# Kernel tuning notes

Hardware: AMD Instinct MI355X
Metric: run time of the kernel (lower is better)

The kernel has to match this reference:

```python
import jax, jax.numpy as jnp
import numpy as np

N = 100_000   # nodes
E = 1_600_000 # edges
D = 128       # feat_dim
H = 128       # hidden dim (both layers)
L = 64        # latent dim
BN_EPS = 1e-5


def setup_inputs() -> dict:
    key = jax.random.key(0)
    ks = jax.random.split(key, 16)
    x = jax.random.normal(ks[0], (N, D), dtype=jnp.float32)
    edge_index = jax.random.randint(ks[1], (2, E), 0, N, dtype=jnp.int64)
    s = 0.05
    return {
        "x": x,
        "edge_index": edge_index,
        # GCN layer 1
        "W1": jax.random.normal(ks[2], (D, H), dtype=jnp.float32) * s,
        "b1": jnp.zeros((H,), dtype=jnp.float32),
        "g1": jnp.ones((H,), dtype=jnp.float32),
        "be1": jnp.zeros((H,), dtype=jnp.float32),
        # GCN layer 2
        "W2": jax.random.normal(ks[3], (H, H), dtype=jnp.float32) * s,
        "b2": jnp.zeros((H,), dtype=jnp.float32),
        "g2": jnp.ones((H,), dtype=jnp.float32),
        "be2": jnp.zeros((H,), dtype=jnp.float32),
        # heads
        "Wmu": jax.random.normal(ks[4], (H, L), dtype=jnp.float32) * s,
        "bmu": jnp.zeros((L,), dtype=jnp.float32),
        "Wlv": jax.random.normal(ks[5], (H, L), dtype=jnp.float32) * s,
        "blv": jnp.zeros((L,), dtype=jnp.float32),
    }


def _gcn_conv(h, src, dst, deg_isqrt, W, b):
    # PyG GCNConv: linear first, then D^{-1/2}(A+I)D^{-1/2} aggregation, then bias.
    hW = h @ W                                   # [N, H]
    norm = deg_isqrt[src] * deg_isqrt[dst]       # [E]
    msg = hW[src] * norm[:, None]                # gather + scale, [E, H]
    agg = jax.ops.segment_sum(msg, dst, num_segments=N)
    # self-loop contribution (norm = deg_isqrt[i]^2)
    agg = agg + hW * (deg_isqrt * deg_isqrt)[:, None]
    return agg + b


def _bn_relu(h, g, be):
    # training-mode BatchNorm1d over the node dim (biased variance), then ReLU
    mean = jnp.mean(h, axis=0)
    var = jnp.mean(jnp.square(h - mean), axis=0)
    hn = (h - mean) * jax.lax.rsqrt(var + BN_EPS) * g + be
    return jax.nn.relu(hn)


def reference(x, edge_index, W1, b1, g1, be1, W2, b2, g2, be2, Wmu, bmu, Wlv, blv):
    src, dst = edge_index[0], edge_index[1]
    # degree with self loops (computed on destination nodes)
    deg = jax.ops.segment_sum(jnp.ones((E,), dtype=x.dtype), dst, num_segments=N) + 1.0
    deg_isqrt = jax.lax.rsqrt(deg)

    h = _bn_relu(_gcn_conv(x, src, dst, deg_isqrt, W1, b1), g1, be1)
    h = _bn_relu(_gcn_conv(h, src, dst, deg_isqrt, W2, b2), g2, be2)
    # dropout is identity in eval mode
    mu = h @ Wmu + bmu
    logvar = h @ Wlv + blv
    return mu, logvar
```

## Files before the change

### kernel.cpp

```cpp
#include <hip/hip_runtime.h>


typedef __attribute__((ext_vector_type(8))) short bf16x8;
typedef __attribute__((ext_vector_type(4))) float f32x4;

#define NB   256
#define PSZ  256
#define PMAX 512

__device__ inline unsigned short f2bf(float f) {
    unsigned u = __float_as_uint(f);
    unsigned r = u + 0x7FFFu + ((u >> 16) & 1u);
    return (unsigned short)(r >> 16);
}
__device__ inline float bf2f(unsigned u16) {
    return __uint_as_float(u16 << 16);
}

__global__ void k_edetect(const int* __restrict__ ei, int n, int* __restrict__ flag) {
    if (threadIdx.x == 0 && blockIdx.x == 0) {
        int is64 = 1;
        for (int i = 0; i < 64; ++i) {
            if (ei[2 * i + 1] != 0 || (unsigned)ei[2 * i] >= (unsigned)n) { is64 = 0; break; }
        }
        *flag = is64;
    }
}

__device__ inline void load_edge(const int* __restrict__ ei, int eflag, size_t i, size_t e,
                                 int& s, int& d) {
    if (eflag) {
        s = ei[2 * i];
        d = ei[2 * e + 2 * i];
    } else {
        s = ei[i];
        d = ei[e + i];
    }
}


__global__ __launch_bounds__(256) void k_hist(const int* __restrict__ ei,
                                              const int* __restrict__ eflag,
                                              unsigned* __restrict__ gh,
                                              int e, int n, int P, int epb) {
    __shared__ unsigned hist[PMAX];
    int t = threadIdx.x, b = blockIdx.x;
    for (int p = t; p < P; p += 256) hist[p] = 0u;
    __syncthreads();
    int f = *eflag;
    int end = min(e, (b + 1) * epb);
    for (int i = b * epb + t; i < end; i += 256) {
        int s, d;
        load_edge(ei, f, (size_t)i, (size_t)e, s, d);
        if ((unsigned)d < (unsigned)n) atomicAdd(&hist[d >> 8], 1u);
    }
    __syncthreads();
    for (int p = t; p < P; p += 256) gh[(size_t)p * NB + b] = hist[p];
}


__global__ __launch_bounds__(256) void k_scanp(const unsigned* __restrict__ gh,
                                               unsigned* __restrict__ boffs,
                                               unsigned* __restrict__ tot, int P) {
    __shared__ unsigned tmp[256];
    int p = blockIdx.x, t = threadIdx.x;
    unsigned v = gh[(size_t)p * NB + t];
    tmp[t] = v;
    __syncthreads();
    for (int o = 1; o < 256; o <<= 1) {
        unsigned u = (t >= o) ? tmp[t - o] : 0u;
        __syncthreads();
        tmp[t] += u;
        __syncthreads();
    }
    boffs[(size_t)p * NB + t] = tmp[t] - v;
    if (t == 255) tot[p] = tmp[255];
}


__global__ void k_scant(const unsigned* __restrict__ tot,
                        unsigned* __restrict__ gofs, int P) {
    __shared__ unsigned tmp[512];
    int t = threadIdx.x;
    unsigned v = (t < P) ? tot[t] : 0u;
    tmp[t] = v;
    __syncthreads();
    for (int o = 1; o < 512; o <<= 1) {
        unsigned u = (t >= o) ? tmp[t - o] : 0u;
        __syncthreads();
        tmp[t] += u;
        __syncthreads();
    }
    if (t < P) gofs[t] = tmp[t] - v;
}


__global__ __launch_bounds__(256) void k_stage(const int* __restrict__ ei,
                                               const int* __restrict__ eflag,
                                               const unsigned* __restrict__ boffs,
                                               const unsigned* __restrict__ gofs,
                                               uint2* __restrict__ staged,
                                               int e, int n, int P, int epb) {
    __shared__ unsigned cur[PMAX];
    int t = threadIdx.x, b = blockIdx.x;
    for (int p = t; p < P; p += 256) cur[p] = gofs[p] + boffs[(size_t)p * NB + b];
    __syncthreads();
    int f = *eflag;
    int end = min(e, (b + 1) * epb);
    for (int i = b * epb + t; i < end; i += 256) {
        int s, d;
        load_edge(ei, f, (size_t)i, (size_t)e, s, d);
        if ((unsigned)d >= (unsigned)n) continue;
        unsigned pos = atomicAdd(&cur[d >> 8], 1u);
        if (pos < (unsigned)e) staged[pos] = make_uint2((unsigned)s, (unsigned)d);
    }
}


__global__ __launch_bounds__(256) void k_fill(const uint2* __restrict__ staged,
                                              const unsigned* __restrict__ gofs,
                                              const unsigned* __restrict__ tot,
                                              int* __restrict__ csr_src,
                                              unsigned* __restrict__ deg,
                                              float* __restrict__ dis,
                                              unsigned* __restrict__ starts,
                                              int n, int P) {
    __shared__ unsigned h2[256], tmp[256], cur2[256];
    int p = blockIdx.x, t = threadIdx.x;
    unsigned base = gofs[p], cnt = tot[p];
    h2[t] = 0u;
    __syncthreads();
    for (unsigned i = t; i < cnt; i += 256) {
        unsigned dl = staged[base + i].y & 255u;
        atomicAdd(&h2[dl], 1u);
    }
    __syncthreads();
    unsigned cv = h2[t];
    tmp[t] = cv;
    __syncthreads();
    for (int o = 1; o < 256; o <<= 1) {
        unsigned u = (t >= o) ? tmp[t - o] : 0u;
        __syncthreads();
        tmp[t] += u;
        __syncthreads();
    }
    unsigned excl = tmp[t] - cv;
    int node = p * PSZ + t;
    if (node < n) {
        deg[node]    = cv;
        dis[node]    = rsqrtf((float)cv + 1.0f);
        starts[node] = base + excl;
    }
    cur2[t] = base + excl;
    __syncthreads();
    for (unsigned i = t; i < cnt; i += 256) {
        uint2 ed = staged[base + i];
        unsigned slot = atomicAdd(&cur2[ed.y & 255u], 1u);
        csr_src[slot] = (ed.x < (unsigned)n) ? (int)ed.x : 0;
    }
}


__global__ __launch_bounds__(256) void prep_weights(const float* __restrict__ W1,
                                                    const float* __restrict__ W2,
                                                    const float* __restrict__ Wmu,
                                                    const float* __restrict__ Wlv,
                                                    const float* __restrict__ bmu,
                                                    const float* __restrict__ blv,
                                                    unsigned short* __restrict__ Wt1,
                                                    unsigned short* __restrict__ Wt2,
                                                    unsigned short* __restrict__ Wtc,
                                                    float* __restrict__ bcat) {
    int idx = blockIdx.x * 256 + threadIdx.x;
    if (idx < 16384) {
        int c = idx >> 7, k = idx & 127;
        Wt1[idx] = f2bf(W1[(size_t)k * 128 + c]);
    } else if (idx < 32768) {
        int t = idx - 16384, c = t >> 7, k = t & 127;
        Wt2[t] = f2bf(W2[(size_t)k * 128 + c]);
    } else if (idx < 49152) {
        int t = idx - 32768, c = t >> 7, k = t & 127;
        float v = (c < 64) ? Wmu[(size_t)k * 64 + c] : Wlv[(size_t)k * 64 + (c - 64)];
        Wtc[t] = f2bf(v);
    }
    if (idx < 128) bcat[idx] = (idx < 64) ? bmu[idx] : blv[idx - 64];
}


__global__ __launch_bounds__(256) void aggregate(const unsigned* __restrict__ hWb,
                                                 const int* __restrict__ csr_src,
                                                 const unsigned* __restrict__ starts,
                                                 const unsigned* __restrict__ deg,
                                                 const float* __restrict__ dis,
                                                 const float* __restrict__ bias,
                                                 float* __restrict__ outh, int n) {
    int node = blockIdx.x * 4 + (threadIdx.x >> 6);
    int lane = threadIdx.x & 63;
    if (node >= n) return;
    unsigned s0 = starts[node], dn = deg[node];
    float ax = 0.f, ay = 0.f;
    unsigned j = 0;
    for (; j + 16 <= dn; j += 16) {
        int si[16]; unsigned vv[16]; float ww[16];
#pragma unroll
        for (int q = 0; q < 16; ++q) si[q] = csr_src[s0 + j + q];
#pragma unroll
        for (int q = 0; q < 16; ++q) vv[q] = hWb[(size_t)si[q] * 64 + lane];
#pragma unroll
        for (int q = 0; q < 16; ++q) ww[q] = dis[si[q]];
#pragma unroll
        for (int q = 0; q < 16; ++q) {
            ax = fmaf(bf2f(vv[q] & 0xFFFFu), ww[q], ax);
            ay = fmaf(bf2f(vv[q] >> 16), ww[q], ay);
        }
    }
    for (; j + 8 <= dn; j += 8) {
        int si[8]; unsigned vv[8]; float ww[8];
#pragma unroll
        for (int q = 0; q < 8; ++q) si[q] = csr_src[s0 + j + q];
#pragma unroll
        for (int q = 0; q < 8; ++q) vv[q] = hWb[(size_t)si[q] * 64 + lane];
#pragma unroll
        for (int q = 0; q < 8; ++q) ww[q] = dis[si[q]];
#pragma unroll
        for (int q = 0; q < 8; ++q) {
            ax = fmaf(bf2f(vv[q] & 0xFFFFu), ww[q], ax);
            ay = fmaf(bf2f(vv[q] >> 16), ww[q], ay);
        }
    }
    for (; j + 4 <= dn; j += 4) {
        int si[4]; unsigned vv[4]; float ww[4];
#pragma unroll
        for (int q = 0; q < 4; ++q) si[q] = csr_src[s0 + j + q];
#pragma unroll
        for (int q = 0; q < 4; ++q) vv[q] = hWb[(size_t)si[q] * 64 + lane];
#pragma unroll
        for (int q = 0; q < 4; ++q) ww[q] = dis[si[q]];
#pragma unroll
        for (int q = 0; q < 4; ++q) {
            ax = fmaf(bf2f(vv[q] & 0xFFFFu), ww[q], ax);
            ay = fmaf(bf2f(vv[q] >> 16), ww[q], ay);
        }
    }
    for (; j < dn; ++j) {
        int      s = csr_src[s0 + j];
        float    w = dis[s];
        unsigned v = hWb[(size_t)s * 64 + lane];
        ax = fmaf(bf2f(v & 0xFFFFu), w, ax);
        ay = fmaf(bf2f(v >> 16), w, ay);
    }
    float dii = dis[node];
    unsigned vs = hWb[(size_t)node * 64 + lane];
    float rx = fmaf(dii, ax, dii * dii * bf2f(vs & 0xFFFFu)) + bias[lane * 2];
    float ry = fmaf(dii, ay, dii * dii * bf2f(vs >> 16)) + bias[lane * 2 + 1];
    *(float2*)(outh + (size_t)node * 128 + lane * 2) = make_float2(rx, ry);
}


__global__ __launch_bounds__(256) void bn_stats(const float* __restrict__ h,
                                                float* __restrict__ sums, int n) {
    int tid = threadIdx.x;
    int c = tid & 127, half = tid >> 7;
    float s = 0.f, s2 = 0.f;
    for (int r = blockIdx.x * 2 + half; r < n; r += gridDim.x * 2) {
        float v = h[(size_t)r * 128 + c];
        s += v;
        s2 = fmaf(v, v, s2);
    }
    __shared__ float sh[256];
    sh[tid] = s;
    __syncthreads();
    if (tid < 128) atomicAdd(&sums[tid], sh[tid] + sh[tid + 128]);
    __syncthreads();
    sh[tid] = s2;
    __syncthreads();
    if (tid < 128) atomicAdd(&sums[128 + tid], sh[tid] + sh[tid + 128]);
}

__global__ void bn_final(const float* __restrict__ sums, const float* __restrict__ g,
                         const float* __restrict__ be, float* __restrict__ bnp, int n) {
    int c = threadIdx.x;
    float inv_n = 1.0f / (float)n;
    float mean = sums[c] * inv_n;
    float var  = sums[128 + c] * inv_n - mean * mean;
    float sc   = g[c] * rsqrtf(var + 1e-5f);
    bnp[c]       = sc;
    bnp[128 + c] = be[c] - mean * sc;
}


template <bool HEAD>
__global__ __launch_bounds__(256, 4) void gemm_mfma(const float* __restrict__ A,
                                                    const unsigned short* __restrict__ Wt,
                                                    const float* __restrict__ bnp,
                                                    const float* __restrict__ bias,
                                                    void* __restrict__ Cv, int nrows) {
    __shared__ float Cl[64][130];
    __shared__ float bnsc[128], bnsh[128];

    const int tid  = threadIdx.x;
    const int lane = tid & 63;
    const int wv   = tid >> 6;
    const int rowbase = blockIdx.x * 64;
    const bool has_bn = (bnp != nullptr);
    if (has_bn && tid < 128) {
        bnsc[tid] = bnp[tid];
        bnsh[tid] = bnp[128 + tid];
    }
    __syncthreads();

    const int ar = rowbase + wv * 16 + (lane & 15);
    const int kg = (lane >> 4) * 8;
    const int bc = lane & 15;

    f32x4 acc[8];
#pragma unroll
    for (int t = 0; t < 8; ++t) acc[t] = {0.f, 0.f, 0.f, 0.f};

#pragma unroll
    for (int k0 = 0; k0 < 128; k0 += 32) {
        float va[8];
        if (ar < nrows) {
            float4 a0 = *(const float4*)(A + (size_t)ar * 128 + k0 + kg);
            float4 a1 = *(const float4*)(A + (size_t)ar * 128 + k0 + kg + 4);
            va[0] = a0.x; va[1] = a0.y; va[2] = a0.z; va[3] = a0.w;
            va[4] = a1.x; va[5] = a1.y; va[6] = a1.z; va[7] = a1.w;
        } else {
#pragma unroll
            for (int i = 0; i < 8; ++i) va[i] = 0.f;
        }
        if (has_bn) {
#pragma unroll
            for (int i = 0; i < 8; ++i) {
                int k = k0 + kg + i;
                va[i] = fmaxf(0.f, fmaf(va[i], bnsc[k], bnsh[k]));
            }
        }
        bf16x8 af;
#pragma unroll
        for (int i = 0; i < 8; ++i) af[i] = (short)f2bf(va[i]);

#pragma unroll
        for (int ct = 0; ct < 8; ++ct) {
            bf16x8 bf = *(const bf16x8*)(Wt + (size_t)(ct * 16 + bc) * 128 + k0 + kg);
            acc[ct] = __builtin_amdgcn_mfma_f32_16x16x32_bf16(af, bf, acc[ct], 0, 0, 0);
        }
    }

    const int lr = wv * 16 + ((lane >> 4) << 2);
#pragma unroll
    for (int ct = 0; ct < 8; ++ct)
#pragma unroll
        for (int r = 0; r < 4; ++r)
            Cl[lr + r][ct * 16 + bc] = acc[ct][r];
    __syncthreads();

    const int row = tid >> 2;
    const int c0  = (tid & 3) * 32;
    const int gr  = rowbase + row;
    if (gr < nrows) {
        if (!HEAD) {
            unsigned* C = (unsigned*)Cv;
#pragma unroll
            for (int u = 0; u < 4; ++u) {
                int cb = c0 + u * 8;
                unsigned o0 = (unsigned)f2bf(Cl[row][cb + 0]) | ((unsigned)f2bf(Cl[row][cb + 1]) << 16);
                unsigned o1 = (unsigned)f2bf(Cl[row][cb + 2]) | ((unsigned)f2bf(Cl[row][cb + 3]) << 16);
                unsigned o2 = (unsigned)f2bf(Cl[row][cb + 4]) | ((unsigned)f2bf(Cl[row][cb + 5]) << 16);
                unsigned o3 = (unsigned)f2bf(Cl[row][cb + 6]) | ((unsigned)f2bf(Cl[row][cb + 7]) << 16);
                uint4 o4 = {o0, o1, o2, o3};
                *(uint4*)(C + (size_t)gr * 64 + cb / 2) = o4;
            }
        } else {
            float* mu = (float*)Cv;
            float* lv = mu + (size_t)nrows * 64;
            float* dst = (c0 < 64) ? (mu + (size_t)gr * 64 + c0) : (lv + (size_t)gr * 64 + (c0 - 64));
#pragma unroll
            for (int u = 0; u < 8; ++u) {
                int cb = c0 + u * 4;
                float4 o = make_float4(Cl[row][cb + 0] + bias[cb + 0],
                                       Cl[row][cb + 1] + bias[cb + 1],
                                       Cl[row][cb + 2] + bias[cb + 2],
                                       Cl[row][cb + 3] + bias[cb + 3]);
                *(float4*)(dst + u * 4) = o;
            }
        }
    }
}


extern "C" void kernel_launch(void* const* d_in, const int* in_sizes, int n_in,
                              void* d_out, int out_size, void* d_ws, size_t ws_size,
                              hipStream_t stream) {
    const float* x   = (const float*)d_in[0];
    const int*   ei  = (const int*)d_in[1];
    const float* W1  = (const float*)d_in[2];
    const float* b1  = (const float*)d_in[3];
    const float* g1  = (const float*)d_in[4];
    const float* be1 = (const float*)d_in[5];
    const float* W2  = (const float*)d_in[6];
    const float* b2  = (const float*)d_in[7];
    const float* g2  = (const float*)d_in[8];
    const float* be2 = (const float*)d_in[9];
    const float* Wmu = (const float*)d_in[10];
    const float* bmu = (const float*)d_in[11];
    const float* Wlv = (const float*)d_in[12];
    const float* blv = (const float*)d_in[13];

    const int n = in_sizes[0] / 128;
    const int e = in_sizes[1] / 2;

    const int P   = (n + PSZ - 1) / PSZ;
    const int epb = (e + NB - 1) / NB;

    char* ws = (char*)d_ws;
    size_t off = 0;
    auto alloc = [&](size_t bytes) {
        void* p = ws + off;
        off = (off + bytes + 255) & ~(size_t)255;
        return p;
    };
    float*          bufH    = (float*)alloc((size_t)n * 128 * 4);
    unsigned*       hWb     = (unsigned*)alloc((size_t)n * 64 * 4);
    uint2*          staged  = (uint2*)alloc((size_t)e * 8);
    int*            csr_src = (int*)alloc((size_t)e * 4);
    unsigned*       gh      = (unsigned*)alloc((size_t)P * NB * 4);
    unsigned*       boffs   = (unsigned*)alloc((size_t)P * NB * 4);
    unsigned*       tot     = (unsigned*)alloc((size_t)P * 4);
    unsigned*       gofs    = (unsigned*)alloc((size_t)P * 4);
    unsigned*       deg     = (unsigned*)alloc((size_t)n * 4);
    float*          dis     = (float*)alloc((size_t)n * 4);
    unsigned*       starts  = (unsigned*)alloc((size_t)n * 4);
    int*            eflag   = (int*)alloc(256);
    float*          sums    = (float*)alloc(256 * 4);
    float*          bnp     = (float*)alloc(256 * 4);
    unsigned short* Wt1     = (unsigned short*)alloc(16384 * 2);
    unsigned short* Wt2     = (unsigned short*)alloc(16384 * 2);
    unsigned short* Wtc     = (unsigned short*)alloc(16384 * 2);
    float*          bcat    = (float*)alloc(128 * 4);

    const int ab = (n + 3) / 4;
    const int gg = (n + 63) / 64;

    prep_weights<<<192, 256, 0, stream>>>(W1, W2, Wmu, Wlv, bmu, blv, Wt1, Wt2, Wtc, bcat);
    k_edetect<<<1, 64, 0, stream>>>(ei, n, eflag);
    k_hist <<<NB, 256, 0, stream>>>(ei, eflag, gh, e, n, P, epb);
    k_scanp<<<P, 256, 0, stream>>>(gh, boffs, tot, P);
    k_scant<<<1, 512, 0, stream>>>(tot, gofs, P);
    k_stage<<<NB, 256, 0, stream>>>(ei, eflag, boffs, gofs, staged, e, n, P, epb);
    k_fill <<<P, 256, 0, stream>>>(staged, gofs, tot, csr_src, deg, dis, starts, n, P);

    gemm_mfma<false><<<gg, 256, 0, stream>>>(x, Wt1, nullptr, nullptr, hWb, n);
    aggregate<<<ab, 256, 0, stream>>>(hWb, csr_src, starts, deg, dis, b1, bufH, n);
    hipMemsetAsync(sums, 0, 1024, stream);
    bn_stats<<<512, 256, 0, stream>>>(bufH, sums, n);
    bn_final<<<1, 128, 0, stream>>>(sums, g1, be1, bnp, n);

    gemm_mfma<false><<<gg, 256, 0, stream>>>(bufH, Wt2, bnp, nullptr, hWb, n);
    aggregate<<<ab, 256, 0, stream>>>(hWb, csr_src, starts, deg, dis, b2, bufH, n);
    hipMemsetAsync(sums, 0, 1024, stream);
    bn_stats<<<512, 256, 0, stream>>>(bufH, sums, n);
    bn_final<<<1, 128, 0, stream>>>(sums, g2, be2, bnp, n);

    gemm_mfma<true><<<gg, 256, 0, stream>>>(bufH, Wtc, bnp, bcat, d_out, n);
}
```

Baseline: 447.5 us.

## Pre-scale GEMM output by source deg^-1/2 and vectorize BN stats

The per-node deg^-1/2 factor is folded into the bf16 output of the feature GEMM, so aggregation becomes a plain sum of gathered rows, with the self term added and a single multiply by the destination factor at the end. This removes the per-edge random gather of dis[src] and the per-edge multiply. Separately, the BatchNorm statistics kernel now reads float4 per thread across 8 row slices and reduces through shared memory. Rounding changes slightly because the scale is applied before bf16 conversion.

```diff
diff --git a/kernel.cpp b/kernel.cpp
--- a/kernel.cpp
+++ b/kernel.cpp
@@ -201,80 +201,85 @@
     float ax = 0.f, ay = 0.f;
     unsigned j = 0;
     for (; j + 16 <= dn; j += 16) {
-        int si[16]; unsigned vv[16]; float ww[16];
+        int si[16]; unsigned vv[16];
 #pragma unroll
         for (int q = 0; q < 16; ++q) si[q] = csr_src[s0 + j + q];
 #pragma unroll
         for (int q = 0; q < 16; ++q) vv[q] = hWb[(size_t)si[q] * 64 + lane];
 #pragma unroll
-        for (int q = 0; q < 16; ++q) ww[q] = dis[si[q]];
-#pragma unroll
         for (int q = 0; q < 16; ++q) {
-            ax = fmaf(bf2f(vv[q] & 0xFFFFu), ww[q], ax);
-            ay = fmaf(bf2f(vv[q] >> 16), ww[q], ay);
+            ax += bf2f(vv[q] & 0xFFFFu);
+            ay += bf2f(vv[q] >> 16);
         }
     }
     for (; j + 8 <= dn; j += 8) {
-        int si[8]; unsigned vv[8]; float ww[8];
+        int si[8]; unsigned vv[8];
 #pragma unroll
         for (int q = 0; q < 8; ++q) si[q] = csr_src[s0 + j + q];
 #pragma unroll
         for (int q = 0; q < 8; ++q) vv[q] = hWb[(size_t)si[q] * 64 + lane];
 #pragma unroll
-        for (int q = 0; q < 8; ++q) ww[q] = dis[si[q]];
-#pragma unroll
         for (int q = 0; q < 8; ++q) {
-            ax = fmaf(bf2f(vv[q] & 0xFFFFu), ww[q], ax);
-            ay = fmaf(bf2f(vv[q] >> 16), ww[q], ay);
+            ax += bf2f(vv[q] & 0xFFFFu);
+            ay += bf2f(vv[q] >> 16);
         }
     }
     for (; j + 4 <= dn; j += 4) {
-        int si[4]; unsigned vv[4]; float ww[4];
+        int si[4]; unsigned vv[4];
 #pragma unroll
         for (int q = 0; q < 4; ++q) si[q] = csr_src[s0 + j + q];
 #pragma unroll
         for (int q = 0; q < 4; ++q) vv[q] = hWb[(size_t)si[q] * 64 + lane];
 #pragma unroll
-        for (int q = 0; q < 4; ++q) ww[q] = dis[si[q]];
-#pragma unroll
         for (int q = 0; q < 4; ++q) {
-            ax = fmaf(bf2f(vv[q] & 0xFFFFu), ww[q], ax);
-            ay = fmaf(bf2f(vv[q] >> 16), ww[q], ay);
+            ax += bf2f(vv[q] & 0xFFFFu);
+            ay += bf2f(vv[q] >> 16);
         }
     }
     for (; j < dn; ++j) {
-        int      s = csr_src[s0 + j];
-        float    w = dis[s];
-        unsigned v = hWb[(size_t)s * 64 + lane];
-        ax = fmaf(bf2f(v & 0xFFFFu), w, ax);
-        ay = fmaf(bf2f(v >> 16), w, ay);
-    }
+        unsigned v = hWb[(size_t)csr_src[s0 + j] * 64 + lane];
+        ax += bf2f(v & 0xFFFFu);
+        ay += bf2f(v >> 16);
+    }
+    unsigned vs = hWb[(size_t)node * 64 + lane];
+    ax += bf2f(vs & 0xFFFFu);
+    ay += bf2f(vs >> 16);
     float dii = dis[node];
-    unsigned vs = hWb[(size_t)node * 64 + lane];
-    float rx = fmaf(dii, ax, dii * dii * bf2f(vs & 0xFFFFu)) + bias[lane * 2];
-    float ry = fmaf(dii, ay, dii * dii * bf2f(vs >> 16)) + bias[lane * 2 + 1];
+    float rx = fmaf(dii, ax, bias[lane * 2]);
+    float ry = fmaf(dii, ay, bias[lane * 2 + 1]);
     *(float2*)(outh + (size_t)node * 128 + lane * 2) = make_float2(rx, ry);
 }
 
 
 __global__ __launch_bounds__(256) void bn_stats(const float* __restrict__ h,
                                                 float* __restrict__ sums, int n) {
-    int tid = threadIdx.x;
-    int c = tid & 127, half = tid >> 7;
-    float s = 0.f, s2 = 0.f;
-    for (int r = blockIdx.x * 2 + half; r < n; r += gridDim.x * 2) {
-        float v = h[(size_t)r * 128 + c];
-        s += v;
-        s2 = fmaf(v, v, s2);
-    }
-    __shared__ float sh[256];
-    sh[tid] = s;
-    __syncthreads();
-    if (tid < 128) atomicAdd(&sums[tid], sh[tid] + sh[tid + 128]);
-    __syncthreads();
-    sh[tid] = s2;
-    __syncthreads();
-    if (tid < 128) atomicAdd(&sums[128 + tid], sh[tid] + sh[tid + 128]);
+    int t  = threadIdx.x;
+    int q  = t & 31;
+    int sl = t >> 5;
+    float s0 = 0.f, s1 = 0.f, s2 = 0.f, s3 = 0.f;
+    float q0 = 0.f, q1 = 0.f, q2 = 0.f, q3 = 0.f;
+    for (int r = blockIdx.x * 8 + sl; r < n; r += gridDim.x * 8) {
+        float4 v = *(const float4*)(h + (size_t)r * 128 + q * 4);
+        s0 += v.x; q0 = fmaf(v.x, v.x, q0);
+        s1 += v.y; q1 = fmaf(v.y, v.y, q1);
+        s2 += v.z; q2 = fmaf(v.z, v.z, q2);
+        s3 += v.w; q3 = fmaf(v.w, v.w, q3);
+    }
+    __shared__ float sh[256][8];
+    sh[t][0] = s0; sh[t][1] = s1; sh[t][2] = s2; sh[t][3] = s3;
+    sh[t][4] = q0; sh[t][5] = q1; sh[t][6] = q2; sh[t][7] = q3;
+    __syncthreads();
+    if (t < 128) {
+        int cq = t >> 2, ce = t & 3;
+        float a = 0.f, b = 0.f;
+#pragma unroll
+        for (int s8 = 0; s8 < 8; ++s8) {
+            a += sh[s8 * 32 + cq][ce];
+            b += sh[s8 * 32 + cq][4 + ce];
+        }
+        atomicAdd(&sums[t], a);
+        atomicAdd(&sums[128 + t], b);
+    }
 }
 
 __global__ void bn_final(const float* __restrict__ sums, const float* __restrict__ g,
@@ -294,6 +299,7 @@
                                                     const unsigned short* __restrict__ Wt,
                                                     const float* __restrict__ bnp,
                                                     const float* __restrict__ bias,
+                                                    const float* __restrict__ disv,
                                                     void* __restrict__ Cv, int nrows) {
     __shared__ float Cl[64][130];
     __shared__ float bnsc[128], bnsh[128];
@@ -360,14 +366,15 @@
     const int gr  = rowbase + row;
     if (gr < nrows) {
         if (!HEAD) {
+            float dsc = disv[gr];
             unsigned* C = (unsigned*)Cv;
 #pragma unroll
             for (int u = 0; u < 4; ++u) {
                 int cb = c0 + u * 8;
-                unsigned o0 = (unsigned)f2bf(Cl[row][cb + 0]) | ((unsigned)f2bf(Cl[row][cb + 1]) << 16);
-                unsigned o1 = (unsigned)f2bf(Cl[row][cb + 2]) | ((unsigned)f2bf(Cl[row][cb + 3]) << 16);
-                unsigned o2 = (unsigned)f2bf(Cl[row][cb + 4]) | ((unsigned)f2bf(Cl[row][cb + 5]) << 16);
-                unsigned o3 = (unsigned)f2bf(Cl[row][cb + 6]) | ((unsigned)f2bf(Cl[row][cb + 7]) << 16);
+                unsigned o0 = (unsigned)f2bf(Cl[row][cb + 0] * dsc) | ((unsigned)f2bf(Cl[row][cb + 1] * dsc) << 16);
+                unsigned o1 = (unsigned)f2bf(Cl[row][cb + 2] * dsc) | ((unsigned)f2bf(Cl[row][cb + 3] * dsc) << 16);
+                unsigned o2 = (unsigned)f2bf(Cl[row][cb + 4] * dsc) | ((unsigned)f2bf(Cl[row][cb + 5] * dsc) << 16);
+                unsigned o3 = (unsigned)f2bf(Cl[row][cb + 6] * dsc) | ((unsigned)f2bf(Cl[row][cb + 7] * dsc) << 16);
                 uint4 o4 = {o0, o1, o2, o3};
                 *(uint4*)(C + (size_t)gr * 64 + cb / 2) = o4;
             }
@@ -450,17 +457,17 @@
     k_stage<<<NB, 256, 0, stream>>>(ei, eflag, boffs, gofs, staged, e, n, P, epb);
     k_fill <<<P, 256, 0, stream>>>(staged, gofs, tot, csr_src, deg, dis, starts, n, P);
 
-    gemm_mfma<false><<<gg, 256, 0, stream>>>(x, Wt1, nullptr, nullptr, hWb, n);
+    gemm_mfma<false><<<gg, 256, 0, stream>>>(x, Wt1, nullptr, nullptr, dis, hWb, n);
     aggregate<<<ab, 256, 0, stream>>>(hWb, csr_src, starts, deg, dis, b1, bufH, n);
     hipMemsetAsync(sums, 0, 1024, stream);
     bn_stats<<<512, 256, 0, stream>>>(bufH, sums, n);
     bn_final<<<1, 128, 0, stream>>>(sums, g1, be1, bnp, n);
 
-    gemm_mfma<false><<<gg, 256, 0, stream>>>(bufH, Wt2, bnp, nullptr, hWb, n);
+    gemm_mfma<false><<<gg, 256, 0, stream>>>(bufH, Wt2, bnp, nullptr, dis, hWb, n);
     aggregate<<<ab, 256, 0, stream>>>(hWb, csr_src, starts, deg, dis, b2, bufH, n);
     hipMemsetAsync(sums, 0, 1024, stream);
     bn_stats<<<512, 256, 0, stream>>>(bufH, sums, n);
     bn_final<<<1, 128, 0, stream>>>(sums, g2, be2, bnp, n);
 
-    gemm_mfma<true><<<gg, 256, 0, stream>>>(bufH, Wtc, bnp, bcat, d_out, n);
-}
+    gemm_mfma<true><<<gg, 256, 0, stream>>>(bufH, Wtc, bnp, bcat, nullptr, d_out, n);
+}
```

Result: faster. 389.3 us (-13.0%).
